# Kernel tuning notes

Measured on AMD Instinct MI355X. Metric: run time of the kernel, lower is better.

## Reference

```python
import jax, jax.numpy as jnp
import numpy as np

NUM_BINS = 256  # must be > max input value (fill_max)

def setup_inputs() -> dict:
    key = jax.random.key(0)
    inputs = jax.random.randint(key, (128, 256, 32, 32), 0, NUM_BINS, dtype=jnp.int32)
    return {"inputs": inputs}

def reference(inputs) -> jnp.ndarray:
    # Faithful to tf: reshape [B,P,S,S] -> [B, P*S*S] (tf.math.bincount flattens
    # its per-map_fn 2D input), per-batch-element histogram, max bin count.
    B = inputs.shape[0]
    flat = inputs.reshape(B, -1)  # [B, N]

    def hist_max(row):
        counts = jnp.zeros((NUM_BINS,), dtype=jnp.int32).at[row].add(1)
        return jnp.max(counts)

    out = jax.vmap(hist_max)(flat)  # [B] int32: mode frequency per batch element
    return out.astype(jnp.float32)
```

## Files before the change

kernel.cpp:

```cpp
#include <hip/hip_runtime.h>


#define NUM_BINS 256
#define NREP     32
#define BLOCK    1024
#define N_PER_B  (256 * 32 * 32)

__global__ __launch_bounds__(BLOCK) void
percolation_fused_kernel(const int* __restrict__ in, float* __restrict__ out) {
    __shared__ int lh[NUM_BINS * NREP];

    for (int i = threadIdx.x; i < NUM_BINS * NREP; i += BLOCK)
        lh[i] = 0;
    __syncthreads();

    const int lane = threadIdx.x & (NREP - 1);

    const int4* p = (const int4*)(in + (size_t)blockIdx.x * N_PER_B);
    const int iters = N_PER_B / 4 / BLOCK;

#pragma unroll 8
    for (int i = 0; i < iters; ++i) {
        int4 v = p[(size_t)i * BLOCK + threadIdx.x];
        atomicAdd(&lh[v.x * NREP + lane], 1);
        atomicAdd(&lh[v.y * NREP + lane], 1);
        atomicAdd(&lh[v.z * NREP + lane], 1);
        atomicAdd(&lh[v.w * NREP + lane], 1);
    }
    __syncthreads();

    int s = 0;
    if (threadIdx.x < NUM_BINS) {
#pragma unroll
        for (int j = 0; j < NREP; ++j)
            s += lh[threadIdx.x * NREP + ((j + threadIdx.x) & (NREP - 1))];
    }

#pragma unroll
    for (int off = 32; off > 0; off >>= 1)
        s = max(s, __shfl_down(s, off, 64));

    __shared__ int wmax[BLOCK / 64];
    if ((threadIdx.x & 63) == 0)
        wmax[threadIdx.x >> 6] = s;
    __syncthreads();

    if (threadIdx.x == 0) {
        int m = wmax[0];
#pragma unroll
        for (int w = 1; w < BLOCK / 64; ++w)
            m = max(m, wmax[w]);
        out[blockIdx.x] = (float)m;
    }
}

extern "C" void kernel_launch(void* const* d_in, const int* in_sizes, int n_in,
                              void* d_out, int out_size, void* d_ws, size_t ws_size,
                              hipStream_t stream) {
    const int* in  = (const int*)d_in[0];
    float*     out = (float*)d_out;
    const int B = out_size;

    percolation_fused_kernel<<<B, BLOCK, 0, stream>>>(in, out);
}
```

Measured before the change: 195.8 us.

## Split each batch histogram across two blocks with cooperative grid sync

Each batch element's histogram is now computed by two blocks, each over half the data. The partial bin counts go to workspace, then after a grid-wide sync the first 128 blocks sum the partials and take the max. This doubles the block count so more compute units take part in the atomic-bound histogram. In exchange it adds a cooperative launch, a grid barrier and a small global round trip for the partials.

```diff
diff --git a/kernel.cpp b/kernel.cpp
--- a/kernel.cpp
+++ b/kernel.cpp
@@ -1,13 +1,20 @@
 #include <hip/hip_runtime.h>
+#include <hip/hip_cooperative_groups.h>
+
+namespace cg = cooperative_groups;
 
 
 #define NUM_BINS 256
 #define NREP     32
+#define BPB      2
 #define BLOCK    1024
 #define N_PER_B  (256 * 32 * 32)
+#define CHUNK    (N_PER_B / BPB)
+#define NBATCH   128
 
 __global__ __launch_bounds__(BLOCK) void
-percolation_fused_kernel(const int* __restrict__ in, float* __restrict__ out) {
+percolation_coop_kernel(const int* __restrict__ in, float* __restrict__ out,
+                        int* __restrict__ part) {
     __shared__ int lh[NUM_BINS * NREP];
 
     for (int i = threadIdx.x; i < NUM_BINS * NREP; i += BLOCK)
@@ -16,8 +23,8 @@
 
     const int lane = threadIdx.x & (NREP - 1);
 
-    const int4* p = (const int4*)(in + (size_t)blockIdx.x * N_PER_B);
-    const int iters = N_PER_B / 4 / BLOCK;
+    const int4* p = (const int4*)(in + (size_t)blockIdx.x * CHUNK);
+    const int iters = CHUNK / 4 / BLOCK;
 
 #pragma unroll 8
     for (int i = 0; i < iters; ++i) {
@@ -29,37 +36,53 @@
     }
     __syncthreads();
 
-    int s = 0;
     if (threadIdx.x < NUM_BINS) {
+        int s = 0;
 #pragma unroll
         for (int j = 0; j < NREP; ++j)
             s += lh[threadIdx.x * NREP + ((j + threadIdx.x) & (NREP - 1))];
+        part[blockIdx.x * NUM_BINS + threadIdx.x] = s;
     }
 
+    cg::this_grid().sync();
+
+    if (blockIdx.x < NBATCH) {
+        int v = 0;
+        if (threadIdx.x < NUM_BINS) {
+            const int* q = part + (size_t)blockIdx.x * BPB * NUM_BINS;
 #pragma unroll
-    for (int off = 32; off > 0; off >>= 1)
-        s = max(s, __shfl_down(s, off, 64));
+            for (int s = 0; s < BPB; ++s)
+                v += q[s * NUM_BINS + threadIdx.x];
+        }
 
-    __shared__ int wmax[BLOCK / 64];
-    if ((threadIdx.x & 63) == 0)
-        wmax[threadIdx.x >> 6] = s;
-    __syncthreads();
+#pragma unroll
+        for (int off = 32; off > 0; off >>= 1)
+            v = max(v, __shfl_down(v, off, 64));
 
-    if (threadIdx.x == 0) {
-        int m = wmax[0];
+        __shared__ int wmax[BLOCK / 64];
+        if ((threadIdx.x & 63) == 0)
+            wmax[threadIdx.x >> 6] = v;
+        __syncthreads();
+
+        if (threadIdx.x == 0) {
+            int m = wmax[0];
 #pragma unroll
-        for (int w = 1; w < BLOCK / 64; ++w)
-            m = max(m, wmax[w]);
-        out[blockIdx.x] = (float)m;
+            for (int w = 1; w < BLOCK / 64; ++w)
+                m = max(m, wmax[w]);
+            out[blockIdx.x] = (float)m;
+        }
     }
 }
 
 extern "C" void kernel_launch(void* const* d_in, const int* in_sizes, int n_in,
                               void* d_out, int out_size, void* d_ws, size_t ws_size,
                               hipStream_t stream) {
-    const int* in  = (const int*)d_in[0];
-    float*     out = (float*)d_out;
-    const int B = out_size;
+    const int* in   = (const int*)d_in[0];
+    float*     out  = (float*)d_out;
+    int*       part = (int*)d_ws;
 
-    percolation_fused_kernel<<<B, BLOCK, 0, stream>>>(in, out);
+    void* args[] = { (void*)&in, (void*)&out, (void*)&part };
+    hipLaunchCooperativeKernel(percolation_coop_kernel,
+                               dim3(NBATCH * BPB), dim3(BLOCK),
+                               args, 0, stream);
 }
```

Measured after the change: 231.2 us. 18.1% more time.
